# Performance work log

Measured on AMD Instinct MI355X. Metric: run time of the kernel, lower is better.

## Reference

```python
import jax, jax.numpy as jnp
import numpy as np

EMB = 768
HEADS = 12
HD = EMB // HEADS
FF = 4 * EMB
EPS = 1e-5


def gelu_tanh(x):
    c = jnp.sqrt(jnp.asarray(2.0 / jnp.pi, x.dtype))
    return 0.5 * x * (1.0 + jnp.tanh(c * (x + 0.044715 * x ** 3)))


def layernorm(x, scale, shift):
    mean = x.mean(-1, keepdims=True)
    var = ((x - mean) ** 2).mean(-1, keepdims=True)
    return scale * (x - mean) / jnp.sqrt(var + EPS) + shift


def setup_inputs() -> dict:
    key = jax.random.key(0)
    ks = jax.random.split(key, 12)
    s = 0.02
    return {
        "x": jax.random.normal(ks[0], (8, 1024, EMB), jnp.float32),
        "Wq": jax.random.normal(ks[1], (EMB, EMB), jnp.float32) * s,
        "Wk": jax.random.normal(ks[2], (EMB, EMB), jnp.float32) * s,
        "Wv": jax.random.normal(ks[3], (EMB, EMB), jnp.float32) * s,
        "Wo": jax.random.normal(ks[4], (EMB, EMB), jnp.float32) * s,
        "bo": jnp.zeros((EMB,), jnp.float32),
        "W1": jax.random.normal(ks[5], (EMB, FF), jnp.float32) * s,
        "b1": jnp.zeros((FF,), jnp.float32),
        "W2": jax.random.normal(ks[6], (FF, EMB), jnp.float32) * s,
        "b2": jnp.zeros((EMB,), jnp.float32),
        "ln1_scale": jnp.ones((EMB,), jnp.float32),
        "ln1_shift": jnp.zeros((EMB,), jnp.float32),
        "ln2_scale": jnp.ones((EMB,), jnp.float32),
        "ln2_shift": jnp.zeros((EMB,), jnp.float32),
    }


def reference(x, Wq, Wk, Wv, Wo, bo, W1, b1, W2, b2,
              ln1_scale, ln1_shift, ln2_scale, ln2_shift):
    B, T, _ = x.shape
    inp = x
    h = layernorm(x, ln1_scale, ln1_shift)
    # QKV projections (no bias, qkv_bias=False)
    q = (h @ Wq).reshape(B, T, HEADS, HD).transpose(0, 2, 1, 3)  # [B,H,T,hd]
    k = (h @ Wk).reshape(B, T, HEADS, HD).transpose(0, 2, 1, 3)
    v = (h @ Wv).reshape(B, T, HEADS, HD).transpose(0, 2, 1, 3)
    scores = jnp.einsum('bhqd,bhkd->bhqk', q, k)
    causal = jnp.triu(jnp.ones((T, T), bool), k=1)
    scores = jnp.where(causal, -jnp.inf, scores)
    attn = jax.nn.softmax(scores / jnp.sqrt(jnp.asarray(HD, x.dtype)), axis=-1)
    ctx = jnp.einsum('bhqk,bhkd->bhqd', attn, v)
    ctx = ctx.transpose(0, 2, 1, 3).reshape(B, T, EMB)
    attn_out = ctx @ Wo + bo
    x = inp + attn_out  # dropout is identity (rate 0 / eval)
    inp = x
    h = layernorm(x, ln2_scale, ln2_shift)
    ff = gelu_tanh(h @ W1 + b1) @ W2 + b2
    return inp + ff
```

## Files before the change

kernel.cpp:

```cpp
#include <hip/hip_runtime.h>
#include <hip/hip_bf16.h>
#include <stdint.h>
#include <stddef.h>

#define EMB 768
#define FFD 3072
#define NHEAD 12
#define HD 64
#define SEQ 1024
#define NTOK 8192
#define QKVW 2304

typedef unsigned short u16;
typedef __attribute__((ext_vector_type(8))) short short8;
typedef __attribute__((ext_vector_type(4))) float f32x4;

__device__ __forceinline__ u16 f2bf(float f) {
  union { float f; uint32_t u; } w; w.f = f;
  uint32_t x = w.u + 0x7fffu + ((w.u >> 16) & 1u);
  return (u16)(x >> 16);
}

__device__ __forceinline__ float bf2f(uint32_t v) {
  union { uint32_t u; float f; } c; c.u = v << 16; return c.f;
}

__device__ __forceinline__ uint32_t pkbf(float lo, float hi) {
  __hip_bfloat162 h = __float22bfloat162_rn(float2{lo, hi});
  union { __hip_bfloat162 h; uint32_t u; } cv; cv.h = h;
  return cv.u;
}

__device__ __forceinline__ void g2l16(const void* g, void* l) {
  __builtin_amdgcn_global_load_lds(
      (const __attribute__((address_space(1))) void*)g,
      (__attribute__((address_space(3))) void*)l, 16, 0, 0);
}

__global__ __launch_bounds__(256)
void transpose_all_kernel(const float* __restrict__ Wq, const float* __restrict__ Wk,
                          const float* __restrict__ Wv, const float* __restrict__ Wo,
                          const float* __restrict__ W1, const float* __restrict__ W2,
                          u16* __restrict__ qkvT, u16* __restrict__ woT,
                          u16* __restrict__ w1T, u16* __restrict__ w2T) {
  __shared__ float tile[32][33];
  const int id = blockIdx.x;
  const float* in; u16* out; int K, N, bx, by;
  if (id < 1728) {
    const int z = id / 576, rem = id % 576;
    in = z == 0 ? Wq : (z == 1 ? Wk : Wv);
    out = qkvT + (size_t)z * EMB * EMB;
    K = EMB; N = EMB; bx = rem % 24; by = rem / 24;
  } else if (id < 2304) {
    const int rem = id - 1728;
    in = Wo; out = woT; K = EMB; N = EMB; bx = rem % 24; by = rem / 24;
  } else if (id < 4608) {
    const int rem = id - 2304;
    in = W1; out = w1T; K = EMB; N = FFD; bx = rem % 96; by = rem / 96;
  } else {
    const int rem = id - 4608;
    in = W2; out = w2T; K = FFD; N = EMB; bx = rem % 24; by = rem / 24;
  }
  const int n0 = bx * 32, k0 = by * 32;
  const int tx = threadIdx.x & 31;
  const int ty = threadIdx.x >> 5;
#pragma unroll
  for (int i = 0; i < 32; i += 8)
    tile[ty + i][tx] = in[(size_t)(k0 + ty + i) * N + n0 + tx];
  __syncthreads();
#pragma unroll
  for (int i = 0; i < 32; i += 8)
    out[(size_t)(n0 + ty + i) * K + k0 + tx] = f2bf(tile[tx][ty + i]);
}

__global__ __launch_bounds__(256)
void ln_vec_kernel(const float* __restrict__ x, const float* __restrict__ sc,
                   const float* __restrict__ sh, u16* __restrict__ out) {
  const int wave = threadIdx.x >> 6, lane = threadIdx.x & 63;
  const int row = blockIdx.x * 4 + wave;
  const float* xr = x + (size_t)row * EMB;
  float4 v[3];
  float s = 0.f, ss = 0.f;
#pragma unroll
  for (int i = 0; i < 3; ++i) {
    v[i] = *(const float4*)(xr + lane * 4 + i * 256);
    s += v[i].x + v[i].y + v[i].z + v[i].w;
    ss += v[i].x * v[i].x + v[i].y * v[i].y + v[i].z * v[i].z + v[i].w * v[i].w;
  }
#pragma unroll
  for (int m = 1; m < 64; m <<= 1) { s += __shfl_xor(s, m, 64); ss += __shfl_xor(ss, m, 64); }
  const float mean = s * (1.f / EMB);
  const float inv = rsqrtf(ss * (1.f / EMB) - mean * mean + 1e-5f);
  u16* orow = out + (size_t)row * EMB;
#pragma unroll
  for (int i = 0; i < 3; ++i) {
    const int c = lane * 4 + i * 256;
    const float4 s4 = *(const float4*)(sc + c);
    const float4 h4 = *(const float4*)(sh + c);
    uint2 w2;
    w2.x = pkbf((v[i].x - mean) * inv * s4.x + h4.x, (v[i].y - mean) * inv * s4.y + h4.y);
    w2.y = pkbf((v[i].z - mean) * inv * s4.z + h4.z, (v[i].w - mean) * inv * s4.w + h4.w);
    *(uint2*)(orow + c) = w2;
  }
}

__global__ __launch_bounds__(256)
void ln_bf_vec_kernel(const u16* __restrict__ x, const float* __restrict__ sc,
                      const float* __restrict__ sh, u16* __restrict__ out) {
  const int wave = threadIdx.x >> 6, lane = threadIdx.x & 63;
  const int row = blockIdx.x * 4 + wave;
  const u16* xr = x + (size_t)row * EMB;
  float v[3][4];
  float s = 0.f, ss = 0.f;
#pragma unroll
  for (int i = 0; i < 3; ++i) {
    const uint2 r2 = *(const uint2*)(xr + lane * 4 + i * 256);
    v[i][0] = bf2f(r2.x & 0xffffu);
    v[i][1] = bf2f(r2.x >> 16);
    v[i][2] = bf2f(r2.y & 0xffffu);
    v[i][3] = bf2f(r2.y >> 16);
#pragma unroll
    for (int j = 0; j < 4; ++j) { s += v[i][j]; ss += v[i][j] * v[i][j]; }
  }
#pragma unroll
  for (int m = 1; m < 64; m <<= 1) { s += __shfl_xor(s, m, 64); ss += __shfl_xor(ss, m, 64); }
  const float mean = s * (1.f / EMB);
  const float inv = rsqrtf(ss * (1.f / EMB) - mean * mean + 1e-5f);
  u16* orow = out + (size_t)row * EMB;
#pragma unroll
  for (int i = 0; i < 3; ++i) {
    const int c = lane * 4 + i * 256;
    const float4 s4 = *(const float4*)(sc + c);
    const float4 h4 = *(const float4*)(sh + c);
    uint2 w2;
    w2.x = pkbf((v[i][0] - mean) * inv * s4.x + h4.x, (v[i][1] - mean) * inv * s4.y + h4.y);
    w2.y = pkbf((v[i][2] - mean) * inv * s4.z + h4.z, (v[i][3] - mean) * inv * s4.w + h4.w);
    *(uint2*)(orow + c) = w2;
  }
}

template <int EPI, int MT, bool SWAP>
__global__ __launch_bounds__(256)
void gemm_kernel(const u16* __restrict__ A, const u16* __restrict__ BT,
                 void* __restrict__ Cp, const float* __restrict__ bias,
                 const float* __restrict__ res, const u16* __restrict__ res16,
                 u16* __restrict__ vTp, int M, int N, int K) {
  constexpr int MI = MT / 32;
  __shared__ u16 As[MT * 64];
  __shared__ u16 Bs[128 * 64];

  const int nwg = gridDim.x * gridDim.y;
  const int orig = blockIdx.y * gridDim.x + blockIdx.x;
  const int swz = (orig & 7) * (nwg >> 3) + (orig >> 3);
  const int m0 = (swz / gridDim.x) * MT;
  const int n0 = (swz % gridDim.x) * 128;

  const int tid = threadIdx.x;
  const int wave = tid >> 6, lane = tid & 63;
  const int wr = wave >> 1, wc = wave & 1;
  const int r = lane & 15, g = lane >> 4;
  const int lrow = lane >> 3;
  const int lelem = (lane & 7) * 8;

  f32x4 acc[MI][4] = {};

  const int nkt = K >> 6;
  for (int kt = 0; kt < nkt; ++kt) {
    const int k0 = kt << 6;
    if (kt) __syncthreads();
#pragma unroll
    for (int q = 0; q < MT / 32; ++q) {
      const int chunk = q * 4 + wave;
      const int row = chunk * 8 + lrow;
      const int e = lelem ^ ((row & 7) << 3);
      g2l16(A + (size_t)(m0 + row) * K + k0 + e, As + chunk * 512);
    }
#pragma unroll
    for (int q = 0; q < 4; ++q) {
      const int chunk = q * 4 + wave;
      const int row = chunk * 8 + lrow;
      const int e = lelem ^ ((row & 7) << 3);
      g2l16(BT + (size_t)(n0 + row) * K + k0 + e, Bs + chunk * 512);
    }
    __syncthreads();
#pragma unroll
    for (int kk = 0; kk < 2; ++kk) {
      short8 af[MI], bf[4];
#pragma unroll
      for (int mi = 0; mi < MI; ++mi) {
        const int row = wr * (MT / 2) + mi * 16 + r;
        af[mi] = *(const short8*)(As + row * 64 + ((kk * 32 + g * 8) ^ ((row & 7) << 3)));
      }
#pragma unroll
      for (int ni = 0; ni < 4; ++ni) {
        const int row = wc * 64 + ni * 16 + r;
        bf[ni] = *(const short8*)(Bs + row * 64 + ((kk * 32 + g * 8) ^ ((row & 7) << 3)));
      }
#pragma unroll
      for (int mi = 0; mi < MI; ++mi)
#pragma unroll
        for (int ni = 0; ni < 4; ++ni) {
          if constexpr (SWAP)
            acc[mi][ni] = __builtin_amdgcn_mfma_f32_16x16x32_bf16(bf[ni], af[mi], acc[mi][ni], 0, 0, 0);
          else
            acc[mi][ni] = __builtin_amdgcn_mfma_f32_16x16x32_bf16(af[mi], bf[ni], acc[mi][ni], 0, 0, 0);
        }
    }
  }

  if constexpr (!SWAP) {
#pragma unroll
    for (int mi = 0; mi < MI; ++mi)
#pragma unroll
      for (int ni = 0; ni < 4; ++ni) {
        const int rowb = m0 + wr * (MT / 2) + mi * 16 + 4 * g;
        const int col = n0 + wc * 64 + ni * 16 + r;
        u16 pk[4];
#pragma unroll
        for (int j = 0; j < 4; ++j) pk[j] = f2bf(acc[mi][ni][j]);
        if (col < 1536) {
#pragma unroll
          for (int j = 0; j < 4; ++j)
            ((u16*)Cp)[(size_t)(rowb + j) * N + col] = pk[j];
        } else {
          uint2 w2;
          w2.x = (uint32_t)pk[0] | ((uint32_t)pk[1] << 16);
          w2.y = (uint32_t)pk[2] | ((uint32_t)pk[3] << 16);
          *(uint2*)(vTp + (size_t)(col - 1536) * NTOK + rowb) = w2;
        }
      }
  } else {
#pragma unroll
    for (int mi = 0; mi < MI; ++mi) {
      const int m = m0 + wr * (MT / 2) + mi * 16 + r;
#pragma unroll
      for (int ni = 0; ni < 4; ++ni) {
        const int nb = n0 + wc * 64 + ni * 16 + 4 * g;
        if constexpr (EPI == 2) {
          const float4 bs = *(const float4*)(bias + nb);
          float tj[4];
#pragma unroll
          for (int j = 0; j < 4; ++j) {
            float t = acc[mi][ni][j] + (&bs.x)[j];
            float e = __expf(1.5957691216057308f * (t + 0.044715f * t * t * t));
            tj[j] = 0.5f * t * (1.f + (1.f - 2.f / (e + 1.f)));
          }
          uint2 w2;
          w2.x = pkbf(tj[0], tj[1]);
          w2.y = pkbf(tj[2], tj[3]);
          *(uint2*)((u16*)Cp + (size_t)m * N + nb) = w2;
        } else if constexpr (EPI == 4) {
          const float4 bs = *(const float4*)(bias + nb);
          const float4 rs = *(const float4*)(res + (size_t)m * N + nb);
          uint2 w2;
          w2.x = pkbf(acc[mi][ni][0] + bs.x + rs.x, acc[mi][ni][1] + bs.y + rs.y);
          w2.y = pkbf(acc[mi][ni][2] + bs.z + rs.z, acc[mi][ni][3] + bs.w + rs.w);
          *(uint2*)((u16*)Cp + (size_t)m * N + nb) = w2;
        } else {
          const float4 bs = *(const float4*)(bias + nb);
          const uint2 r2 = *(const uint2*)(res16 + (size_t)m * N + nb);
          float4 o;
          o.x = acc[mi][ni][0] + bs.x + bf2f(r2.x & 0xffffu);
          o.y = acc[mi][ni][1] + bs.y + bf2f(r2.x >> 16);
          o.z = acc[mi][ni][2] + bs.z + bf2f(r2.y & 0xffffu);
          o.w = acc[mi][ni][3] + bs.w + bf2f(r2.y >> 16);
          *(float4*)((float*)Cp + (size_t)m * N + nb) = o;
        }
      }
    }
  }
}

#define CEXP 0.18033688011112042f

__global__ __launch_bounds__(256, 3)
void attn_kernel(const u16* __restrict__ qkv, const u16* __restrict__ vT,
                 u16* __restrict__ ctx) {
  const int bh = blockIdx.x;
  const int qt = blockIdx.y;
  const int b = bh / NHEAD, h = bh % NHEAD;
  const int tid = threadIdx.x;
  const int wave = tid >> 6, lane = tid & 63;
  const int r = lane & 15, g = lane >> 4;

  __shared__ u16 Kb[2][64 * 64];
  __shared__ u16 Vb[2][64 * 64];
  __shared__ u16 Pt[4][16 * 64];

  const int qw = qt * 128 + wave * 32;
  const int tok0 = b * SEQ;

  short8 aq[2][2];
#pragma unroll
  for (int qf = 0; qf < 2; ++qf) {
    const u16* qb = qkv + (size_t)(tok0 + qw + qf * 16 + r) * QKVW + h * HD;
    aq[qf][0] = *(const short8*)(qb + g * 8);
    aq[qf][1] = *(const short8*)(qb + 32 + g * 8);
  }

  float l_st[2] = {0.f, 0.f};
  f32x4 oc[2][4] = {};

  const int sr = tid >> 3;
  const int sc = (tid & 7) * 8;
  const int nt = 2 * qt + 2;

  const u16* kg = qkv + (size_t)tok0 * QKVW + EMB + h * HD;
  const u16* vg = vT + (size_t)(h * HD) * NTOK + tok0;
  const int e0 = sc ^ ((sr & 7) << 3);

  auto stage = [&](int buf, int kt) {
    const size_t koff = (size_t)kt * 64;
    u16* kb = (u16*)Kb[buf] + wave * 512;
    u16* vb = (u16*)Vb[buf] + wave * 512;
    g2l16(kg + (koff + sr) * QKVW + e0, kb);
    g2l16(kg + (koff + sr + 32) * QKVW + e0, kb + 2048);
    g2l16(vg + (size_t)sr * NTOK + koff + e0, vb);
    g2l16(vg + (size_t)(sr + 32) * NTOK + koff + e0, vb + 2048);
  };

  stage(0, 0);
  for (int kb = 0; kb < nt; ++kb) {
    __syncthreads();
    const int cur = kb & 1;
    if (kb + 1 < nt) stage(cur ^ 1, kb + 1);

    const int kv0 = kb * 64;
    if (kv0 > qw + 31) continue;

    short8 kf[4][2];
#pragma unroll
    for (int nf = 0; nf < 4; ++nf) {
      const int row = nf * 16 + r;
#pragma unroll
      for (int kk = 0; kk < 2; ++kk)
        kf[nf][kk] = *(const short8*)((char*)Kb[cur] + row * 128 +
                                      ((kk * 64 + g * 16) ^ ((row & 7) << 4)));
    }
    short8 bv[2][4];
#pragma unroll
    for (int half = 0; half < 2; ++half)
#pragma unroll
      for (int nd = 0; nd < 4; ++nd) {
        const int vr = nd * 16 + r;
        bv[half][nd] = *(const short8*)((char*)Vb[cur] + vr * 128 +
                       ((half * 64 + g * 16) ^ ((vr & 7) << 4)));
      }

#pragma unroll
    for (int qf = 0; qf < 2; ++qf) {
      f32x4 st[4];
#pragma unroll
      for (int nf = 0; nf < 4; ++nf) {
        f32x4 z = {};
        z = __builtin_amdgcn_mfma_f32_16x16x32_bf16(kf[nf][0], aq[qf][0], z, 0, 0, 0);
        z = __builtin_amdgcn_mfma_f32_16x16x32_bf16(kf[nf][1], aq[qf][1], z, 0, 0, 0);
        st[nf] = z;
      }
      if (kv0 + 63 > qw + qf * 16) {
        const int qg = qw + qf * 16 + r;
#pragma unroll
        for (int nf = 0; nf < 4; ++nf)
#pragma unroll
          for (int j = 0; j < 4; ++j)
            if (kv0 + nf * 16 + 4 * g + j > qg) st[nf][j] = -3e38f;
      }
      float p[4][4];
      float ps = 0.f;
#pragma unroll
      for (int nf = 0; nf < 4; ++nf)
#pragma unroll
        for (int j = 0; j < 4; ++j) {
          const float pe = exp2f(st[nf][j] * CEXP);
          p[nf][j] = pe;
          ps += pe;
        }
      ps += __shfl_xor(ps, 16);
      ps += __shfl_xor(ps, 32);
      l_st[qf] += ps;

      u16* Pw = (u16*)Pt[wave];
#pragma unroll
      for (int nf = 0; nf < 4; ++nf) {
        uint2 w2;
        w2.x = pkbf(p[nf][0], p[nf][1]);
        w2.y = pkbf(p[nf][2], p[nf][3]);
        *(uint2*)((char*)Pw + r * 128 + ((nf * 32 + g * 8) ^ ((r & 7) << 4))) = w2;
      }
#pragma unroll
      for (int half = 0; half < 2; ++half) {
        short8 pa = *(const short8*)((char*)Pw + r * 128 +
                                     ((half * 64 + g * 16) ^ ((r & 7) << 4)));
#pragma unroll
        for (int nd = 0; nd < 4; ++nd)
          oc[qf][nd] = __builtin_amdgcn_mfma_f32_16x16x32_bf16(pa, bv[half][nd], oc[qf][nd], 0, 0, 0);
      }
    }
  }

#pragma unroll
  for (int qf = 0; qf < 2; ++qf) {
    const float rl = 1.f / l_st[qf];
#pragma unroll
    for (int j = 0; j < 4; ++j) {
      const float rj = __shfl(rl, 4 * g + j, 16);
      const size_t row = (size_t)tok0 + qw + qf * 16 + 4 * g + j;
#pragma unroll
      for (int nd = 0; nd < 4; ++nd)
        ctx[row * EMB + h * HD + nd * 16 + r] = f2bf(oc[qf][nd][j] * rj);
    }
  }
}

extern "C" void kernel_launch(void* const* d_in, const int* in_sizes, int n_in,
                              void* d_out, int out_size, void* d_ws, size_t ws_size,
                              hipStream_t stream) {
  const float* x    = (const float*)d_in[0];
  const float* Wq   = (const float*)d_in[1];
  const float* Wk   = (const float*)d_in[2];
  const float* Wv   = (const float*)d_in[3];
  const float* Wo   = (const float*)d_in[4];
  const float* bo   = (const float*)d_in[5];
  const float* W1   = (const float*)d_in[6];
  const float* b1   = (const float*)d_in[7];
  const float* W2   = (const float*)d_in[8];
  const float* b2   = (const float*)d_in[9];
  const float* ln1s = (const float*)d_in[10];
  const float* ln1b = (const float*)d_in[11];
  const float* ln2s = (const float*)d_in[12];
  const float* ln2b = (const float*)d_in[13];

  char* p = (char*)d_ws;
  u16* qkvT = (u16*)p; p += (size_t)QKVW * EMB * 2;
  u16* woT  = (u16*)p; p += (size_t)EMB * EMB * 2;
  u16* w1T  = (u16*)p; p += (size_t)FFD * EMB * 2;
  u16* w2T  = (u16*)p; p += (size_t)EMB * FFD * 2;
  u16* h1   = (u16*)p; p += (size_t)NTOK * EMB * 2;
  u16* qkv  = (u16*)p; p += (size_t)NTOK * QKVW * 2;
  u16* x2bf = (u16*)p; p += (size_t)NTOK * EMB * 2;
  u16* ff1  = (u16*)p; p += (size_t)NTOK * FFD * 2;
  u16* ctxb = h1;
  u16* h2   = qkv;
  u16* vT   = ff1;

  if (ws_size < (size_t)(p - (char*)d_ws)) return;

  dim3 blk(256);
  transpose_all_kernel<<<6912, blk, 0, stream>>>(Wq, Wk, Wv, Wo, W1, W2, qkvT, woT, w1T, w2T);
  ln_vec_kernel<<<NTOK / 4, blk, 0, stream>>>(x, ln1s, ln1b, h1);
  gemm_kernel<3, 128, false><<<dim3(18, 64), blk, 0, stream>>>(h1, qkvT, qkv, nullptr, nullptr, nullptr, vT, NTOK, QKVW, EMB);
  attn_kernel<<<dim3(96, 8), blk, 0, stream>>>(qkv, vT, ctxb);
  gemm_kernel<4, 64, true><<<dim3(6, 128), blk, 0, stream>>>(ctxb, woT, x2bf, bo, x, nullptr, nullptr, NTOK, EMB, EMB);
  ln_bf_vec_kernel<<<NTOK / 4, blk, 0, stream>>>(x2bf, ln2s, ln2b, h2);
  gemm_kernel<2, 128, true><<<dim3(24, 64), blk, 0, stream>>>(h2, w1T, ff1, b1, nullptr, nullptr, nullptr, NTOK, FFD, EMB);
  gemm_kernel<5, 64, true><<<dim3(6, 128), blk, 0, stream>>>(ff1, w2T, (float*)d_out, b2, nullptr, x2bf, nullptr, NTOK, EMB, FFD);
}
```

Measured before the change: 221.6 us.

## Double-buffer GEMM K-tiles and merge LayerNorm1 into weight prep kernel

The GEMM main loop now uses two LDS buffers with a K-step of 32 and issues the global-to-LDS loads for the next tile before computing the current one. This aims to hide load latency behind MFMA work while keeping LDS use the same. Separately, the first LayerNorm is folded into the weight transpose kernel as extra blocks, which saves one kernel launch. The cost is twice as many barriers per K, and each barrier now covers only half as many MFMAs.

```diff
diff --git a/kernel.cpp b/kernel.cpp
--- a/kernel.cpp
+++ b/kernel.cpp
@@ -38,13 +38,44 @@
 }
 
 __global__ __launch_bounds__(256)
-void transpose_all_kernel(const float* __restrict__ Wq, const float* __restrict__ Wk,
-                          const float* __restrict__ Wv, const float* __restrict__ Wo,
-                          const float* __restrict__ W1, const float* __restrict__ W2,
-                          u16* __restrict__ qkvT, u16* __restrict__ woT,
-                          u16* __restrict__ w1T, u16* __restrict__ w2T) {
+void prep_kernel(const float* __restrict__ Wq, const float* __restrict__ Wk,
+                 const float* __restrict__ Wv, const float* __restrict__ Wo,
+                 const float* __restrict__ W1, const float* __restrict__ W2,
+                 u16* __restrict__ qkvT, u16* __restrict__ woT,
+                 u16* __restrict__ w1T, u16* __restrict__ w2T,
+                 const float* __restrict__ x, const float* __restrict__ sc,
+                 const float* __restrict__ sh, u16* __restrict__ h1) {
   __shared__ float tile[32][33];
   const int id = blockIdx.x;
+  if (id >= 6912) {
+    const int wave = threadIdx.x >> 6, lane = threadIdx.x & 63;
+    const int row = (id - 6912) * 4 + wave;
+    const float* xr = x + (size_t)row * EMB;
+    float4 v[3];
+    float s = 0.f, ss = 0.f;
+#pragma unroll
+    for (int i = 0; i < 3; ++i) {
+      v[i] = *(const float4*)(xr + lane * 4 + i * 256);
+      s += v[i].x + v[i].y + v[i].z + v[i].w;
+      ss += v[i].x * v[i].x + v[i].y * v[i].y + v[i].z * v[i].z + v[i].w * v[i].w;
+    }
+#pragma unroll
+    for (int m = 1; m < 64; m <<= 1) { s += __shfl_xor(s, m, 64); ss += __shfl_xor(ss, m, 64); }
+    const float mean = s * (1.f / EMB);
+    const float inv = rsqrtf(ss * (1.f / EMB) - mean * mean + 1e-5f);
+    u16* orow = h1 + (size_t)row * EMB;
+#pragma unroll
+    for (int i = 0; i < 3; ++i) {
+      const int c = lane * 4 + i * 256;
+      const float4 s4 = *(const float4*)(sc + c);
+      const float4 h4 = *(const float4*)(sh + c);
+      uint2 w2;
+      w2.x = pkbf((v[i].x - mean) * inv * s4.x + h4.x, (v[i].y - mean) * inv * s4.y + h4.y);
+      w2.y = pkbf((v[i].z - mean) * inv * s4.z + h4.z, (v[i].w - mean) * inv * s4.w + h4.w);
+      *(uint2*)(orow + c) = w2;
+    }
+    return;
+  }
   const float* in; u16* out; int K, N, bx, by;
   if (id < 1728) {
     const int z = id / 576, rem = id % 576;
@@ -74,37 +105,6 @@
 }
 
 __global__ __launch_bounds__(256)
-void ln_vec_kernel(const float* __restrict__ x, const float* __restrict__ sc,
-                   const float* __restrict__ sh, u16* __restrict__ out) {
-  const int wave = threadIdx.x >> 6, lane = threadIdx.x & 63;
-  const int row = blockIdx.x * 4 + wave;
-  const float* xr = x + (size_t)row * EMB;
-  float4 v[3];
-  float s = 0.f, ss = 0.f;
-#pragma unroll
-  for (int i = 0; i < 3; ++i) {
-    v[i] = *(const float4*)(xr + lane * 4 + i * 256);
-    s += v[i].x + v[i].y + v[i].z + v[i].w;
-    ss += v[i].x * v[i].x + v[i].y * v[i].y + v[i].z * v[i].z + v[i].w * v[i].w;
-  }
-#pragma unroll
-  for (int m = 1; m < 64; m <<= 1) { s += __shfl_xor(s, m, 64); ss += __shfl_xor(ss, m, 64); }
-  const float mean = s * (1.f / EMB);
-  const float inv = rsqrtf(ss * (1.f / EMB) - mean * mean + 1e-5f);
-  u16* orow = out + (size_t)row * EMB;
-#pragma unroll
-  for (int i = 0; i < 3; ++i) {
-    const int c = lane * 4 + i * 256;
-    const float4 s4 = *(const float4*)(sc + c);
-    const float4 h4 = *(const float4*)(sh + c);
-    uint2 w2;
-    w2.x = pkbf((v[i].x - mean) * inv * s4.x + h4.x, (v[i].y - mean) * inv * s4.y + h4.y);
-    w2.y = pkbf((v[i].z - mean) * inv * s4.z + h4.z, (v[i].w - mean) * inv * s4.w + h4.w);
-    *(uint2*)(orow + c) = w2;
-  }
-}
-
-__global__ __launch_bounds__(256)
 void ln_bf_vec_kernel(const u16* __restrict__ x, const float* __restrict__ sc,
                       const float* __restrict__ sh, u16* __restrict__ out) {
   const int wave = threadIdx.x >> 6, lane = threadIdx.x & 63;
@@ -146,8 +146,8 @@
                  const float* __restrict__ res, const u16* __restrict__ res16,
                  u16* __restrict__ vTp, int M, int N, int K) {
   constexpr int MI = MT / 32;
-  __shared__ u16 As[MT * 64];
-  __shared__ u16 Bs[128 * 64];
+  __shared__ u16 As[2][MT * 32];
+  __shared__ u16 Bs[2][128 * 32];
 
   const int nwg = gridDim.x * gridDim.y;
   const int orig = blockIdx.y * gridDim.x + blockIdx.x;
@@ -159,53 +159,51 @@
   const int wave = tid >> 6, lane = tid & 63;
   const int wr = wave >> 1, wc = wave & 1;
   const int r = lane & 15, g = lane >> 4;
-  const int lrow = lane >> 3;
-  const int lelem = (lane & 7) * 8;
+  const int strow = wave * 16 + (lane >> 2);
+  const int e0 = ((lane & 3) * 8) ^ ((strow & 3) << 3);
 
   f32x4 acc[MI][4] = {};
 
-  const int nkt = K >> 6;
+  auto stage = [&](int buf, int kt) {
+    const int k0 = kt << 5;
+#pragma unroll
+    for (int ra = 0; ra < MT / 64; ++ra)
+      g2l16(A + (size_t)(m0 + ra * 64 + strow) * K + k0 + e0,
+            (u16*)As[buf] + ra * 2048 + wave * 512);
+#pragma unroll
+    for (int rb = 0; rb < 2; ++rb)
+      g2l16(BT + (size_t)(n0 + rb * 64 + strow) * K + k0 + e0,
+            (u16*)Bs[buf] + rb * 2048 + wave * 512);
+  };
+
+  const int nkt = K >> 5;
+  stage(0, 0);
   for (int kt = 0; kt < nkt; ++kt) {
-    const int k0 = kt << 6;
-    if (kt) __syncthreads();
-#pragma unroll
-    for (int q = 0; q < MT / 32; ++q) {
-      const int chunk = q * 4 + wave;
-      const int row = chunk * 8 + lrow;
-      const int e = lelem ^ ((row & 7) << 3);
-      g2l16(A + (size_t)(m0 + row) * K + k0 + e, As + chunk * 512);
-    }
-#pragma unroll
-    for (int q = 0; q < 4; ++q) {
-      const int chunk = q * 4 + wave;
-      const int row = chunk * 8 + lrow;
-      const int e = lelem ^ ((row & 7) << 3);
-      g2l16(BT + (size_t)(n0 + row) * K + k0 + e, Bs + chunk * 512);
-    }
     __syncthreads();
-#pragma unroll
-    for (int kk = 0; kk < 2; ++kk) {
-      short8 af[MI], bf[4];
-#pragma unroll
-      for (int mi = 0; mi < MI; ++mi) {
-        const int row = wr * (MT / 2) + mi * 16 + r;
-        af[mi] = *(const short8*)(As + row * 64 + ((kk * 32 + g * 8) ^ ((row & 7) << 3)));
-      }
+    const int cur = kt & 1;
+    if (kt + 1 < nkt) stage(cur ^ 1, kt + 1);
+    const u16* ab = (const u16*)As[cur];
+    const u16* bb = (const u16*)Bs[cur];
+    short8 af[MI], bf[4];
+#pragma unroll
+    for (int mi = 0; mi < MI; ++mi) {
+      const int row = wr * (MT / 2) + mi * 16 + r;
+      af[mi] = *(const short8*)(ab + row * 32 + ((g * 8) ^ ((row & 3) << 3)));
+    }
+#pragma unroll
+    for (int ni = 0; ni < 4; ++ni) {
+      const int row = wc * 64 + ni * 16 + r;
+      bf[ni] = *(const short8*)(bb + row * 32 + ((g * 8) ^ ((row & 3) << 3)));
+    }
+#pragma unroll
+    for (int mi = 0; mi < MI; ++mi)
 #pragma unroll
       for (int ni = 0; ni < 4; ++ni) {
-        const int row = wc * 64 + ni * 16 + r;
-        bf[ni] = *(const short8*)(Bs + row * 64 + ((kk * 32 + g * 8) ^ ((row & 7) << 3)));
-      }
-#pragma unroll
-      for (int mi = 0; mi < MI; ++mi)
-#pragma unroll
-        for (int ni = 0; ni < 4; ++ni) {
-          if constexpr (SWAP)
-            acc[mi][ni] = __builtin_amdgcn_mfma_f32_16x16x32_bf16(bf[ni], af[mi], acc[mi][ni], 0, 0, 0);
-          else
-            acc[mi][ni] = __builtin_amdgcn_mfma_f32_16x16x32_bf16(af[mi], bf[ni], acc[mi][ni], 0, 0, 0);
-        }
-    }
+        if constexpr (SWAP)
+          acc[mi][ni] = __builtin_amdgcn_mfma_f32_16x16x32_bf16(bf[ni], af[mi], acc[mi][ni], 0, 0, 0);
+        else
+          acc[mi][ni] = __builtin_amdgcn_mfma_f32_16x16x32_bf16(af[mi], bf[ni], acc[mi][ni], 0, 0, 0);
+      }
   }
 
   if constexpr (!SWAP) {
@@ -446,8 +444,8 @@
   if (ws_size < (size_t)(p - (char*)d_ws)) return;
 
   dim3 blk(256);
-  transpose_all_kernel<<<6912, blk, 0, stream>>>(Wq, Wk, Wv, Wo, W1, W2, qkvT, woT, w1T, w2T);
-  ln_vec_kernel<<<NTOK / 4, blk, 0, stream>>>(x, ln1s, ln1b, h1);
+  prep_kernel<<<8960, blk, 0, stream>>>(Wq, Wk, Wv, Wo, W1, W2, qkvT, woT, w1T, w2T,
+                                        x, ln1s, ln1b, h1);
   gemm_kernel<3, 128, false><<<dim3(18, 64), blk, 0, stream>>>(h1, qkvT, qkv, nullptr, nullptr, nullptr, vT, NTOK, QKVW, EMB);
   attn_kernel<<<dim3(96, 8), blk, 0, stream>>>(qkv, vT, ctxb);
   gemm_kernel<4, 64, true><<<dim3(6, 128), blk, 0, stream>>>(ctxb, woT, x2bf, bo, x, nullptr, nullptr, NTOK, EMB, EMB);
```

New measurement: 280.2 us. 26.4% more time.
